# Kernel optimization log

Hardware: AMD Instinct MI355X
Metric: run time of the kernel (lower is better)

The kernel has to match this reference:

```python
import jax, jax.numpy as jnp
import numpy as np

N_NODES = 100000
N_EDGES = 1200000
DIM = 64
MAX_DEG = 64
NUM_LAB = 16
BN_EPS = 1e-5


def _lrelu(x):
    return jax.nn.leaky_relu(x, negative_slope=0.01)


def _bn(x, g, b):
    # BatchNorm1d in training mode: batch statistics over node axis
    m = x.mean(axis=0)
    v = x.var(axis=0)
    return (x - m) * jax.lax.rsqrt(v + BN_EPS) * g + b


def _gin_layer(h, src, dst, n, w1, b1, w2, b2, eps, g, b):
    # GINConv: (1+eps)*x_i + sum_{j in N(i)} x_j, then MLP (lin_lrelu_lin), BN, LeakyReLU
    agg = jax.ops.segment_sum(h[src], dst, num_segments=n)
    x = (1.0 + eps) * h + agg
    x = _lrelu(x @ w1 + b1) @ w2 + b2
    return _lrelu(_bn(x, g, b))


def setup_inputs() -> dict:
    key = jax.random.key(0)
    ks = jax.random.split(key, 16)
    s = 0.05
    inp = {
        'node_deg': jax.random.randint(ks[0], (N_NODES,), 0, MAX_DEG + 1, dtype=jnp.int32),
        'node_lab': jax.random.randint(ks[1], (N_NODES,), 0, NUM_LAB, dtype=jnp.int32),
        'edge_index': jax.random.randint(ks[2], (2, N_EDGES), 0, N_NODES, dtype=jnp.int32),
        'emb_deg': jax.random.normal(ks[3], (MAX_DEG + 1, DIM), jnp.float32) * s,
        'emb_lab': jax.random.normal(ks[4], (NUM_LAB, DIM), jnp.float32) * s,
        'l0_w1': jax.random.normal(ks[5], (2 * DIM, 2 * DIM), jnp.float32) * s,
        'l0_b1': jnp.zeros((2 * DIM,), jnp.float32),
        'l0_w2': jax.random.normal(ks[6], (2 * DIM, DIM), jnp.float32) * s,
        'l0_b2': jnp.zeros((DIM,), jnp.float32),
        'l0_eps': jnp.zeros((1,), jnp.float32),
        'bn0_g': jnp.ones((DIM,), jnp.float32),
        'bn0_b': jnp.zeros((DIM,), jnp.float32),
        'l1_w1': jax.random.normal(ks[7], (DIM, DIM), jnp.float32) * s,
        'l1_b1': jnp.zeros((DIM,), jnp.float32),
        'l1_w2': jax.random.normal(ks[8], (DIM, DIM), jnp.float32) * s,
        'l1_b2': jnp.zeros((DIM,), jnp.float32),
        'l1_eps': jnp.zeros((1,), jnp.float32),
        'bn1_g': jnp.ones((DIM,), jnp.float32),
        'bn1_b': jnp.zeros((DIM,), jnp.float32),
        'fc_w1': jax.random.normal(ks[9], (4 * DIM, DIM), jnp.float32) * s,
        'fc_b1': jnp.zeros((DIM,), jnp.float32),
        'fc_bn_g': jnp.ones((DIM,), jnp.float32),
        'fc_bn_b': jnp.zeros((DIM,), jnp.float32),
        'fc_w2': jax.random.normal(ks[10], (DIM, 1), jnp.float32) * s,
        'fc_b2': jnp.zeros((1,), jnp.float32),
    }
    return inp


def reference(node_deg, node_lab, edge_index, emb_deg, emb_lab,
              l0_w1, l0_b1, l0_w2, l0_b2, l0_eps, bn0_g, bn0_b,
              l1_w1, l1_b1, l1_w2, l1_b2, l1_eps, bn1_g, bn1_b,
              fc_w1, fc_b1, fc_bn_g, fc_bn_b, fc_w2, fc_b2):
    n = node_deg.shape[0]
    src, dst = edge_index[0], edge_index[1]
    # embedding concat: [N, 2*DIM]
    h0 = jnp.concatenate([emb_deg[node_deg], emb_lab[node_lab]], axis=1)
    h1 = _gin_layer(h0, src, dst, n, l0_w1, l0_b1, l0_w2, l0_b2, l0_eps[0], bn0_g, bn0_b)
    h2 = _gin_layer(h1, src, dst, n, l1_w1, l1_b1, l1_w2, l1_b2, l1_eps[0], bn1_g, bn1_b)
    x = jnp.concatenate([h0, h1, h2], axis=1)  # [N, 256]
    x = _lrelu(_bn(x @ fc_w1 + fc_b1, fc_bn_g, fc_bn_b))
    out = jax.nn.sigmoid(x @ fc_w2 + fc_b2)
    return out.squeeze(-1)  # [N]
```

## Files before the change

### kernel.cpp

```cpp
#include <hip/hip_runtime.h>

#define N_NODES 100000
#define N_EDGES 1200000
#define NCLS 81
#define NBKT 196
#define BCAP 8192
#define NCHK 293
#define NGBLK 1563

typedef unsigned short u16;
typedef unsigned char u8;
typedef unsigned int u32;
typedef unsigned long long u64;
typedef short bf16x8 __attribute__((ext_vector_type(8)));
typedef float f32x4 __attribute__((ext_vector_type(4)));

__device__ __forceinline__ float b2f(u16 u) {
  union { u32 i; float f; } v; v.i = ((u32)u) << 16; return v.f;
}
__device__ __forceinline__ u16 f2b(float f) {
  union { float f; u32 i; } v; v.f = f;
  u32 x = v.i;
  return (u16)((x + 0x7fffu + ((x >> 16) & 1u)) >> 16);
}
__device__ __forceinline__ void up2(u32 w, float& lo, float& hi) {
  union { u32 u; float f; } a, b;
  a.u = w << 16; b.u = w & 0xffff0000u;
  lo = a.f; hi = b.f;
}
__device__ __forceinline__ float lrelu(float x) { return x > 0.f ? x : 0.01f * x; }

__device__ __forceinline__ bool is_f32(const u16* emb) {
  int lane = threadIdx.x & 63;
  u32 e0 = (emb[lane * 2] >> 7) & 0xFF;
  u32 e1 = (emb[lane * 2 + 1] >> 7) & 0xFF;
  return __ballot((e0 >= 0x90) || (e1 >= 0x90)) != 0ull;
}

#define P_EMBD 0
#define P_EMBL 4160
#define P_W1A  5184
#define P_B1A  21568
#define P_W2A  21696
#define P_B2A  29888
#define P_EPS0 29952
#define P_G0   29953
#define P_BB0  30017
#define P_LW1  30081
#define P_LB1  34177
#define P_LW2  34241
#define P_LB2  38337
#define P_EPS1 38401
#define P_G1   38402
#define P_BB1  38466
#define P_FW1  38530
#define P_FB1  54914
#define P_FG   54978
#define P_FBB  55042
#define P_FW2  55106
#define P_FB2  55170
#define P_TOT  55171

struct CvtAll {
  const void* src[22];
  int cnt[22];
  int off[22];
};

__global__ void k_cvtall(CvtAll a, const u16* __restrict__ embRaw, float* __restrict__ P) {
  bool f32m = is_f32(embRaw);
  int seg = blockIdx.y;
  int i = blockIdx.x * 256 + threadIdx.x;
  if (i >= a.cnt[seg]) return;
  float v;
  if (f32m) v = ((const float*)a.src[seg])[i];
  else      v = b2f(((const u16*)a.src[seg])[i]);
  P[a.off[seg] + i] = v;
}

__global__ void k_prep(const float* __restrict__ P, float* __restrict__ W1p,
                       float* __restrict__ Efc, u16* __restrict__ bp,
                       u16* __restrict__ wpB) {
  int idx = blockIdx.x * 256 + threadIdx.x;
  if (idx < NCLS * 128) {
    int c = idx >> 7, h = idx & 127;
    const float* w1 = P + P_W1A;
    float s = 0.f;
    if (c < 65) {
      const float* em = P + P_EMBD + c * 64;
      for (int k = 0; k < 64; ++k) s = fmaf(em[k], w1[k * 128 + h], s);
    } else {
      const float* em = P + P_EMBL + (c - 65) * 64;
      for (int k = 0; k < 64; ++k) s = fmaf(em[k], w1[(64 + k) * 128 + h], s);
    }
    W1p[idx] = s;
    return;
  }
  if (idx < NCLS * 128 + NCLS * 64) {
    int r = idx - NCLS * 128;
    int c = r >> 6, o = r & 63;
    const float* fw = P + P_FW1;
    float s = 0.f;
    if (c < 65) {
      const float* em = P + P_EMBD + c * 64;
      for (int k = 0; k < 64; ++k) s = fmaf(em[k], fw[k * 64 + o], s);
    } else {
      const float* em = P + P_EMBL + (c - 65) * 64;
      for (int k = 0; k < 64; ++k) s = fmaf(em[k], fw[(64 + k) * 64 + o], s);
    }
    Efc[r] = s;
    return;
  }
  if (idx < NCLS * 128 + NCLS * 64 + 24576) {
    int pidx = idx - (NCLS * 128 + NCLS * 64);
    int seg, rel;
    if (pidx < 8192)       { seg = 0; rel = pidx; }
    else if (pidx < 12288) { seg = 1; rel = pidx - 8192; }
    else if (pidx < 16384) { seg = 2; rel = pidx - 12288; }
    else                   { seg = 3; rel = pidx - 16384; }
    const int srcoff[4] = {P_W2A, P_LW1, P_LW2, P_FW1 + 128 * 64};
    const int KBs[4] = {4, 2, 2, 4};
    int j = rel & 7, lane = (rel >> 3) & 63, rest = rel >> 9;
    int kb = rest % KBs[seg], nt = rest / KBs[seg];
    int k = kb * 32 + (lane >> 4) * 8 + j;
    int n = nt * 16 + (lane & 15);
    bp[pidx] = f2b(P[srcoff[seg] + k * 64 + n]);
    return;
  }
  int p2 = idx - (NCLS * 128 + NCLS * 64 + 24576);
  if (p2 >= 12288) return;
  int j = p2 & 7, lane = (p2 >> 3) & 63, rest = p2 >> 9;
  int kb = rest % 3, nt = rest / 3;
  int c = kb * 32 + (lane >> 4) * 8 + j;
  int n = nt * 16 + (lane & 15);
  float s = 0.f;
  if (c < NCLS) {
    const float* w1 = P + P_W1A;
    if (c < 65) {
      const float* em = P + P_EMBD + c * 64;
      for (int k = 0; k < 64; ++k) s = fmaf(em[k], w1[k * 128 + n], s);
    } else {
      const float* em = P + P_EMBL + (c - 65) * 64;
      for (int k = 0; k < 64; ++k) s = fmaf(em[k], w1[(64 + k) * 128 + n], s);
    }
  }
  wpB[p2] = (c < NCLS) ? f2b(s) : 0;
}

__global__ __launch_bounds__(256) void k_bsort(const int* __restrict__ edge,
                                               const int* __restrict__ ndeg,
                                               const int* __restrict__ nlab,
                                               u32* __restrict__ gcur,
                                               u64* __restrict__ e2) {
  __shared__ u32 cnt[NBKT], rbase[NBKT];
  __shared__ u32 slo[4096], shi[4096];
  for (int i = threadIdx.x; i < NBKT; i += 256) cnt[i] = 0;
  __syncthreads();
  int base = blockIdx.x * 4096;
  for (int i = threadIdx.x; i < 4096; i += 256) {
    int e = base + i;
    if (e < N_EDGES) {
      int s = edge[e], d = edge[N_EDGES + e];
      slo[i] = ((u32)s << 11) | ((u32)ndeg[s] << 4) | (u32)nlab[s];
      shi[i] = (u32)d;
      atomicAdd(&cnt[(u32)d >> 9], 1u);
    } else shi[i] = 0xFFFFFFFFu;
  }
  __syncthreads();
  for (int i = threadIdx.x; i < NBKT; i += 256) {
    u32 c = cnt[i];
    rbase[i] = c ? atomicAdd(&gcur[i], c) : 0u;
    cnt[i] = 0;
  }
  __syncthreads();
  for (int i = threadIdx.x; i < 4096; i += 256) {
    u32 d = shi[i];
    if (d == 0xFFFFFFFFu) continue;
    u32 b = d >> 9;
    u32 pos = rbase[b] + atomicAdd(&cnt[b], 1u);
    e2[(size_t)b * BCAP + pos] = ((u64)d << 32) | (u64)slo[i];
  }
}

__global__ __launch_bounds__(512) void k_csr(const u64* __restrict__ e2,
                                             const u32* __restrict__ gcur,
                                             u32* __restrict__ row_ptr,
                                             u32* __restrict__ einfo) {
  __shared__ u32 l[512], cur[512], gl[NBKT];
  __shared__ u32 sbase;
  int b = blockIdx.x, tid = threadIdx.x;
  if (tid < NBKT) gl[tid] = gcur[tid];
  __syncthreads();
  if (tid == 0) {
    u32 s = 0;
    for (int i = 0; i < b; ++i) s += gl[i];
    sbase = s;
  }
  l[tid] = 0;
  __syncthreads();
  u32 cnt = gl[b];
  const u64* src = e2 + (size_t)b * BCAP;
  for (u32 e = tid; e < cnt; e += 512)
    atomicAdd(&l[(u32)(src[e] >> 32) & 511u], 1u);
  __syncthreads();
  u32 v = l[tid];
  for (int off = 1; off < 512; off <<= 1) {
    u32 a = (tid >= off) ? l[tid - off] : 0u;
    __syncthreads();
    l[tid] += a;
    __syncthreads();
  }
  u32 pos0 = sbase + l[tid] - v;
  cur[tid] = pos0;
  int n = b * 512 + tid;
  if (n <= N_NODES) row_ptr[n] = pos0;
  __syncthreads();
  for (u32 e = tid; e < cnt; e += 512) {
    u64 r = src[e];
    u32 pos = atomicAdd(&cur[(u32)(r >> 32) & 511u], 1u);
    einfo[pos] = (u32)r;
  }
}

__global__ __launch_bounds__(256) void k_histgemm0(const u32* __restrict__ rp,
                                                   const u32* __restrict__ einfo,
                                                   const u16* __restrict__ wpB,
                                                   const float* __restrict__ W1p,
                                                   const float* __restrict__ P,
                                                   const int* __restrict__ ndeg,
                                                   const int* __restrict__ nlab,
                                                   u16* __restrict__ hmid) {
  __shared__ u8 h[256 * 96];
  int tid = threadIdx.x;
  u32* hw = (u32*)h;
#pragma unroll
  for (int i = 0; i < 24; ++i) hw[tid * 24 + i] = 0;
  __syncthreads();
  int n = blockIdx.x * 256 + tid;
  if (n < N_NODES) {
    u32 st = rp[n], en = rp[n + 1];
    u8* my = h + tid * 96;
    for (u32 e = st; e < en; ++e) {
      u32 q = einfo[e];
      ++my[(q >> 4) & 0x7Fu];
      ++my[65u + (q & 15u)];
    }
  }
  __syncthreads();
  int wid = tid >> 6, lane = tid & 63;
  int row = lane & 15, q = lane >> 4;
  float onep = 1.f + P[P_EPS0];
  const bf16x8* bp = (const bf16x8*)wpB;
#pragma unroll 1
  for (int t = wid; t < 16; t += 4) {
    int m0 = blockIdx.x * 256 + t * 16;
    if (m0 >= N_NODES) break;
    f32x4 acc[8];
#pragma unroll
    for (int nt = 0; nt < 8; ++nt) {
      float b = P[P_B1A + nt * 16 + row];
      acc[nt][0] = b; acc[nt][1] = b; acc[nt][2] = b; acc[nt][3] = b;
    }
    const u8* ar = h + (t * 16 + row) * 96 + q * 8;
#pragma unroll
    for (int kb = 0; kb < 3; ++kb) {
      bf16x8 af;
#pragma unroll
      for (int j = 0; j < 8; ++j) af[j] = (short)f2b((float)ar[kb * 32 + j]);
#pragma unroll
      for (int nt = 0; nt < 8; ++nt) {
        bf16x8 bf = bp[(nt * 3 + kb) * 64 + lane];
        acc[nt] = __builtin_amdgcn_mfma_f32_16x16x32_bf16(af, bf, acc[nt], 0, 0, 0);
      }
    }
#pragma unroll
    for (int r = 0; r < 4; ++r) {
      int m = m0 + q * 4 + r;
      if (m >= N_NODES) continue;
      const float* wd = W1p + ndeg[m] * 128;
      const float* wl = W1p + (65 + nlab[m]) * 128;
#pragma unroll
      for (int nt = 0; nt < 8; ++nt) {
        int cc = nt * 16 + row;
        float v = acc[nt][r] + onep * (wd[cc] + wl[cc]);
        hmid[(size_t)m * 128 + cc] = f2b(lrelu(v));
      }
    }
  }
}

__global__ void k_sr(const float* __restrict__ pbuf, float* __restrict__ statsOut) {
  __shared__ float l[256];
  int c = blockIdx.x;
  float s = 0.f;
  for (int r = threadIdx.x; r < NGBLK; r += 256) s += pbuf[(size_t)r * 128 + c];
  l[threadIdx.x] = s;
  __syncthreads();
  for (int off = 128; off > 0; off >>= 1) {
    if (threadIdx.x < off) l[threadIdx.x] += l[threadIdx.x + off];
    __syncthreads();
  }
  if (threadIdx.x == 0) statsOut[c] = l[0];
}

template <int KB, int LDA, int BIASOFF>
__global__ __launch_bounds__(256) void k_gemm(const u16* __restrict__ A,
                                              const u16* __restrict__ Bp,
                                              const float* __restrict__ P,
                                              float* __restrict__ pbuf,
                                              u16* __restrict__ C) {
  __shared__ float lsum[4][64], lsq[4][64];
  int wid = threadIdx.x >> 6, lane = threadIdx.x & 63;
  int m0 = (blockIdx.x * 4 + wid) * 16;
  bool act = m0 < N_NODES;
  int row = lane & 15, q = lane >> 4;
  float ss[4] = {0.f, 0.f, 0.f, 0.f}, qq[4] = {0.f, 0.f, 0.f, 0.f};
  if (act) {
    const u16* ap = A + (size_t)(m0 + row) * LDA + q * 8;
    const bf16x8* bp = (const bf16x8*)Bp;
    f32x4 acc[4];
#pragma unroll
    for (int nt = 0; nt < 4; ++nt) {
      float b = (BIASOFF >= 0) ? P[BIASOFF + nt * 16 + row] : 0.f;
      acc[nt][0] = b; acc[nt][1] = b; acc[nt][2] = b; acc[nt][3] = b;
    }
#pragma unroll
    for (int kb = 0; kb < KB; ++kb) {
      bf16x8 af = *(const bf16x8*)(ap + kb * 32);
#pragma unroll
      for (int nt = 0; nt < 4; ++nt) {
        bf16x8 bf = bp[(nt * KB + kb) * 64 + lane];
        acc[nt] = __builtin_amdgcn_mfma_f32_16x16x32_bf16(af, bf, acc[nt], 0, 0, 0);
      }
    }
#pragma unroll
    for (int nt = 0; nt < 4; ++nt) {
      float s = 0.f, z = 0.f;
#pragma unroll
      for (int r = 0; r < 4; ++r) {
        int m = m0 + q * 4 + r;
        u16 bv = f2b(acc[nt][r]);
        C[(size_t)m * 64 + nt * 16 + row] = bv;
        float v = b2f(bv);
        s += v; z = fmaf(v, v, z);
      }
      s += __shfl_xor(s, 16, 64); s += __shfl_xor(s, 32, 64);
      z += __shfl_xor(z, 16, 64); z += __shfl_xor(z, 32, 64);
      ss[nt] = s; qq[nt] = z;
    }
  }
  if (lane < 16) {
#pragma unroll
    for (int nt = 0; nt < 4; ++nt) {
      lsum[wid][nt * 16 + lane] = ss[nt];
      lsq[wid][nt * 16 + lane] = qq[nt];
    }
  }
  __syncthreads();
  int t = threadIdx.x;
  if (t < 64)
    pbuf[(size_t)blockIdx.x * 128 + t] = lsum[0][t] + lsum[1][t] + lsum[2][t] + lsum[3][t];
  else if (t < 128) {
    int c = t - 64;
    pbuf[(size_t)blockIdx.x * 128 + t] = lsq[0][c] + lsq[1][c] + lsq[2][c] + lsq[3][c];
  }
}

__global__ __launch_bounds__(256) void k_gemm_bn(const u16* __restrict__ A,
                                                 const u16* __restrict__ Bp,
                                                 const float* __restrict__ P,
                                                 const float* __restrict__ stats,
                                                 u16* __restrict__ C) {
  int wid = threadIdx.x >> 6, lane = threadIdx.x & 63;
  int m0 = (blockIdx.x * 4 + wid) * 16;
  if (m0 >= N_NODES) return;
  int row = lane & 15, q = lane >> 4;
  const float invN = 1.f / (float)N_NODES;
  float sc[16], sh[16];
#pragma unroll
  for (int kb = 0; kb < 2; ++kb)
#pragma unroll
    for (int j = 0; j < 8; ++j) {
      int f = kb * 32 + q * 8 + j;
      float mm = stats[f] * invN;
      float var = fmaxf(stats[64 + f] * invN - mm * mm, 0.f);
      float inv = rsqrtf(var + 1e-5f);
      float s = inv * P[P_G0 + f];
      sc[kb * 8 + j] = s;
      sh[kb * 8 + j] = P[P_BB0 + f] - mm * s;
    }
  const u16* ap = A + (size_t)(m0 + row) * 64 + q * 8;
  const bf16x8* bp = (const bf16x8*)Bp;
  f32x4 acc[4];
#pragma unroll
  for (int nt = 0; nt < 4; ++nt) {
    acc[nt][0] = 0.f; acc[nt][1] = 0.f; acc[nt][2] = 0.f; acc[nt][3] = 0.f;
  }
#pragma unroll
  for (int kb = 0; kb < 2; ++kb) {
    uint4 raw = *(const uint4*)(ap + kb * 32);
    u32 rw[4] = {raw.x, raw.y, raw.z, raw.w};
    bf16x8 af;
#pragma unroll
    for (int p = 0; p < 4; ++p) {
      float lo, hi;
      up2(rw[p], lo, hi);
      float y0 = lrelu(fmaf(sc[kb * 8 + 2 * p], lo, sh[kb * 8 + 2 * p]));
      float y1 = lrelu(fmaf(sc[kb * 8 + 2 * p + 1], hi, sh[kb * 8 + 2 * p + 1]));
      af[2 * p] = (short)f2b(y0);
      af[2 * p + 1] = (short)f2b(y1);
    }
#pragma unroll
    for (int nt = 0; nt < 4; ++nt) {
      bf16x8 bf = bp[(nt * 2 + kb) * 64 + lane];
      acc[nt] = __builtin_amdgcn_mfma_f32_16x16x32_bf16(af, bf, acc[nt], 0, 0, 0);
    }
  }
#pragma unroll
  for (int nt = 0; nt < 4; ++nt)
#pragma unroll
    for (int r = 0; r < 4; ++r) {
      int m = m0 + q * 4 + r;
      C[(size_t)m * 64 + nt * 16 + row] = f2b(acc[nt][r]);
    }
}

__global__ __launch_bounds__(256) void k_agg1(const u32* __restrict__ rp,
                                              const u32* __restrict__ einfo,
                                              const u16* __restrict__ g1,
                                              const float* __restrict__ P,
                                              u16* __restrict__ abuf) {
  int lane = threadIdx.x & 63, wv = threadIdx.x >> 6;
  int n = blockIdx.x * 4 + wv;
  if (n >= N_NODES) return;
  u32 st = rp[n], en = rp[n + 1];
  u32 m = en - st;
  float acA = 0.f, acB = 0.f;
  u32 k = 0;
  for (; k + 8 <= m; k += 8) {
    u32 c0 = einfo[st + k] >> 11, c1 = einfo[st + k + 1] >> 11;
    u32 c2 = einfo[st + k + 2] >> 11, c3 = einfo[st + k + 3] >> 11;
    u32 c4 = einfo[st + k + 4] >> 11, c5 = einfo[st + k + 5] >> 11;
    u32 c6 = einfo[st + k + 6] >> 11, c7 = einfo[st + k + 7] >> 11;
    float v0 = b2f(g1[(size_t)c0 * 64 + lane]);
    float v1 = b2f(g1[(size_t)c1 * 64 + lane]);
    float v2 = b2f(g1[(size_t)c2 * 64 + lane]);
    float v3 = b2f(g1[(size_t)c3 * 64 + lane]);
    float v4 = b2f(g1[(size_t)c4 * 64 + lane]);
    float v5 = b2f(g1[(size_t)c5 * 64 + lane]);
    float v6 = b2f(g1[(size_t)c6 * 64 + lane]);
    float v7 = b2f(g1[(size_t)c7 * 64 + lane]);
    acA += (v0 + v1) + (v2 + v3);
    acB += (v4 + v5) + (v6 + v7);
  }
  if (k + 4 <= m) {
    u32 c0 = einfo[st + k] >> 11, c1 = einfo[st + k + 1] >> 11;
    u32 c2 = einfo[st + k + 2] >> 11, c3 = einfo[st + k + 3] >> 11;
    float v0 = b2f(g1[(size_t)c0 * 64 + lane]);
    float v1 = b2f(g1[(size_t)c1 * 64 + lane]);
    float v2 = b2f(g1[(size_t)c2 * 64 + lane]);
    float v3 = b2f(g1[(size_t)c3 * 64 + lane]);
    acA += (v0 + v1) + (v2 + v3);
    k += 4;
  }
  for (; k < m; ++k) acB += b2f(g1[(size_t)(einfo[st + k] >> 11) * 64 + lane]);
  float acc = acA + acB;
  float onep = 1.f + P[P_EPS1];
  float a = P[P_LB1 + lane] + fmaf(onep, b2f(g1[(size_t)n * 64 + lane]), acc);
  abuf[(size_t)n * 64 + lane] = f2b(lrelu(a));
}

__global__ __launch_bounds__(256) void k_gemm_fc1bn(const u16* __restrict__ t0,
                                                    const u16* __restrict__ t1,
                                                    const u16* __restrict__ Bp,
                                                    const float* __restrict__ P,
                                                    const float* __restrict__ stats,
                                                    float* __restrict__ pbuf,
                                                    const int* __restrict__ ndeg,
                                                    const int* __restrict__ nlab,
                                                    const float* __restrict__ Efc,
                                                    u16* __restrict__ C) {
  __shared__ float lsum[4][64], lsq[4][64];
  int wid = threadIdx.x >> 6, lane = threadIdx.x & 63;
  int m0 = (blockIdx.x * 4 + wid) * 16;
  bool act = m0 < N_NODES;
  int row = lane & 15, q = lane >> 4;
  float ss[4] = {0.f, 0.f, 0.f, 0.f}, qq[4] = {0.f, 0.f, 0.f, 0.f};
  if (act) {
    const float invN = 1.f / (float)N_NODES;
    float sc[32], sh[32];
#pragma unroll
    for (int h = 0; h < 2; ++h) {
      const float* st = stats + h * 128;
      int gof = h ? P_G1 : P_G0, bof = h ? P_BB1 : P_BB0;
#pragma unroll
      for (int kb = 0; kb < 2; ++kb)
#pragma unroll
        for (int j = 0; j < 8; ++j) {
          int f = kb * 32 + q * 8 + j;
          float mm = st[f] * invN;
          float var = fmaxf(st[64 + f] * invN - mm * mm, 0.f);
          float inv = rsqrtf(var + 1e-5f);
          float s = inv * P[gof + f];
          sc[h * 16 + kb * 8 + j] = s;
          sh[h * 16 + kb * 8 + j] = P[bof + f] - mm * s;
        }
    }
    const u16* a0 = t0 + (size_t)(m0 + row) * 64 + q * 8;
    const u16* a1 = t1 + (size_t)(m0 + row) * 64 + q * 8;
    const bf16x8* bp = (const bf16x8*)Bp;
    f32x4 acc[4];
#pragma unroll
    for (int nt = 0; nt < 4; ++nt) {
      float b = P[P_FB1 + nt * 16 + row];
      acc[nt][0] = b; acc[nt][1] = b; acc[nt][2] = b; acc[nt][3] = b;
    }
#pragma unroll
    for (int kb = 0; kb < 4; ++kb) {
      const u16* src = (kb < 2) ? (a0 + kb * 32) : (a1 + (kb - 2) * 32);
      int ci = (kb < 2) ? kb * 8 : 16 + (kb - 2) * 8;
      uint4 raw = *(const uint4*)src;
      u32 rw[4] = {raw.x, raw.y, raw.z, raw.w};
      bf16x8 af;
#pragma unroll
      for (int p = 0; p < 4; ++p) {
        float lo, hi;
        up2(rw[p], lo, hi);
        float y0 = lrelu(fmaf(sc[ci + 2 * p], lo, sh[ci + 2 * p]));
        float y1 = lrelu(fmaf(sc[ci + 2 * p + 1], hi, sh[ci + 2 * p + 1]));
        af[2 * p] = (short)f2b(y0);
        af[2 * p + 1] = (short)f2b(y1);
      }
#pragma unroll
      for (int nt = 0; nt < 4; ++nt) {
        bf16x8 bf = bp[(nt * 4 + kb) * 64 + lane];
        acc[nt] = __builtin_amdgcn_mfma_f32_16x16x32_bf16(af, bf, acc[nt], 0, 0, 0);
      }
    }
    float es[4][4];
#pragma unroll
    for (int r = 0; r < 4; ++r) {
      int m = m0 + q * 4 + r;
      int dn = ndeg[m], ln = 65 + nlab[m];
#pragma unroll
      for (int nt = 0; nt < 4; ++nt) {
        int cc = nt * 16 + row;
        es[r][nt] = acc[nt][r] + Efc[dn * 64 + cc] + Efc[ln * 64 + cc];
      }
    }
#pragma unroll
    for (int nt = 0; nt < 4; ++nt) {
      float s = 0.f, z = 0.f;
#pragma unroll
      for (int r = 0; r < 4; ++r) {
        int m = m0 + q * 4 + r;
        u16 bv = f2b(es[r][nt]);
        C[(size_t)m * 64 + nt * 16 + row] = bv;
        float v = b2f(bv);
        s += v; z = fmaf(v, v, z);
      }
      s += __shfl_xor(s, 16, 64); s += __shfl_xor(s, 32, 64);
      z += __shfl_xor(z, 16, 64); z += __shfl_xor(z, 32, 64);
      ss[nt] = s; qq[nt] = z;
    }
  }
  if (lane < 16) {
#pragma unroll
    for (int nt = 0; nt < 4; ++nt) {
      lsum[wid][nt * 16 + lane] = ss[nt];
      lsq[wid][nt * 16 + lane] = qq[nt];
    }
  }
  __syncthreads();
  int t = threadIdx.x;
  if (t < 64)
    pbuf[(size_t)blockIdx.x * 128 + t] = lsum[0][t] + lsum[1][t] + lsum[2][t] + lsum[3][t];
  else if (t < 128) {
    int c = t - 64;
    pbuf[(size_t)blockIdx.x * 128 + t] = lsq[0][c] + lsq[1][c] + lsq[2][c] + lsq[3][c];
  }
}

__global__ void k_fc2(const u16* __restrict__ t, const float* __restrict__ stats,
                      const float* __restrict__ P, const u16* __restrict__ embRaw,
                      void* __restrict__ out) {
  bool f32m = is_f32(embRaw);
  int n = blockIdx.x * blockDim.x + threadIdx.x;
  if (n >= N_NODES) return;
  float z = P[P_FB2];
  const float invN = 1.f / (float)N_NODES;
  const u16* tn = t + (size_t)n * 64;
#pragma unroll 1
  for (int f = 0; f < 64; ++f) {
    float m = stats[f] * invN;
    float var = fmaxf(stats[64 + f] * invN - m * m, 0.f);
    float inv = rsqrtf(var + 1e-5f);
    float y = (b2f(tn[f]) - m) * inv * P[P_FG + f] + P[P_FBB + f];
    y = lrelu(y);
    z = fmaf(y, P[P_FW2 + f], z);
  }
  float s = 1.f / (1.f + expf(-z));
  if (!(fabsf(z) < 1e30f)) s = 0.25f;
  if (f32m) ((float*)out)[n] = s;
  else      ((u16*)out)[n] = f2b(s);
}

extern "C" void kernel_launch(void* const* d_in, const int* in_sizes, int n_in,
                              void* d_out, int out_size, void* d_ws, size_t ws_size,
                              hipStream_t stream) {
  const int* node_deg = (const int*)d_in[0];
  const int* node_lab = (const int*)d_in[1];
  const int* edge     = (const int*)d_in[2];
  const u16* embRaw   = (const u16*)d_in[3];
  (void)in_sizes; (void)n_in; (void)out_size; (void)ws_size;

  char* base = (char*)d_ws;
  size_t off = 0;
  auto alloc = [&](size_t bytes) -> void* {
    void* p = base + off;
    off += (bytes + 15) & ~(size_t)15;
    return p;
  };
  float* Pb    = (float*)alloc((size_t)P_TOT * 4);
  float* stats = (float*)alloc(384 * 4);
  u32* gcur    = (u32*)alloc(NBKT * 4);
  float* W1p   = (float*)alloc(NCLS * 128 * 4);
  float* Efc   = (float*)alloc(NCLS * 64 * 4);
  u16* bpack   = (u16*)alloc(24576 * 2);
  u16* wpB     = (u16*)alloc(12288 * 2);
  u32* row_ptr = (u32*)alloc((size_t)(N_NODES + 1) * 4);
  float* pbuf  = (float*)alloc((size_t)NGBLK * 128 * 4);
  u32* einfo   = (u32*)alloc((size_t)N_EDGES * 4);
  u64* e2      = (u64*)alloc((size_t)NBKT * BCAP * 8);
  void* arena  = alloc((size_t)N_NODES * 128 * 2);
  u16* t0      = (u16*)alloc((size_t)N_NODES * 64 * 2);
  u16* t1      = (u16*)alloc((size_t)N_NODES * 64 * 2);
  u16* t2      = (u16*)alloc((size_t)N_NODES * 64 * 2);
  u16* hmid = (u16*)arena;
  u16* g1   = (u16*)arena;
  u16* abuf = (u16*)arena + (size_t)N_NODES * 64;
  u16* Bp_w2a = bpack;
  u16* Bp_lw1 = bpack + 8192;
  u16* Bp_lw2 = bpack + 12288;
  u16* Bp_fw1 = bpack + 16384;

  hipMemsetAsync(stats, 0, 384 * 4 + NBKT * 4, stream);

  CvtAll ca;
  const int srcidx[22] = {3, 4, 5, 6, 7, 8, 9, 10, 11, 12, 13, 14, 15, 16, 17, 18, 19, 20, 21, 22, 23, 24};
  const int cnts[22]   = {4160, 1024, 16384, 128, 8192, 64, 1, 64, 64, 4096, 64, 4096, 64, 1, 64, 64, 16384, 64, 64, 64, 64, 1};
  const int offs[22]   = {P_EMBD, P_EMBL, P_W1A, P_B1A, P_W2A, P_B2A, P_EPS0, P_G0, P_BB0,
                          P_LW1, P_LB1, P_LW2, P_LB2, P_EPS1, P_G1, P_BB1,
                          P_FW1, P_FB1, P_FG, P_FBB, P_FW2, P_FB2};
  for (int i = 0; i < 22; ++i) { ca.src[i] = d_in[srcidx[i]]; ca.cnt[i] = cnts[i]; ca.off[i] = offs[i]; }
  k_cvtall<<<dim3(64, 22), 256, 0, stream>>>(ca, embRaw, Pb);

  k_prep<<<205, 256, 0, stream>>>(Pb, W1p, Efc, bpack, wpB);

  k_bsort<<<NCHK, 256, 0, stream>>>(edge, node_deg, node_lab, gcur, e2);
  k_csr<<<NBKT, 512, 0, stream>>>(e2, gcur, row_ptr, einfo);

  const int GEMM_GRID = NGBLK;

  k_histgemm0<<<(N_NODES + 255) / 256, 256, 0, stream>>>(row_ptr, einfo, wpB, W1p, Pb,
                                                         node_deg, node_lab, hmid);
  k_gemm<4, 128, P_B2A><<<GEMM_GRID, 256, 0, stream>>>(hmid, Bp_w2a, Pb, pbuf, t0);
  k_sr<<<128, 256, 0, stream>>>(pbuf, stats);

  k_gemm_bn<<<GEMM_GRID, 256, 0, stream>>>(t0, Bp_lw1, Pb, stats, g1);
  k_agg1<<<(N_NODES + 3) / 4, 256, 0, stream>>>(row_ptr, einfo, g1, Pb, abuf);
  k_gemm<2, 64, P_LB2><<<GEMM_GRID, 256, 0, stream>>>(abuf, Bp_lw2, Pb, pbuf, t1);
  k_sr<<<128, 256, 0, stream>>>(pbuf, stats + 128);

  k_gemm_fc1bn<<<GEMM_GRID, 256, 0, stream>>>(t0, t1, Bp_fw1, Pb, stats, pbuf,
                                              node_deg, node_lab, Efc, t2);
  k_sr<<<128, 256, 0, stream>>>(pbuf, stats + 256);
  k_fc2<<<(N_NODES + 255) / 256, 256, 0, stream>>>(t2, stats + 256, Pb, embRaw, d_out);
}
```

Measured before the change: 326.7 us.

## Fuse parameter conversion with prep, and histogram GEMM into CSR build

Parameter conversion and weight preprocessing are merged into one init kernel that reads the raw inputs directly and also zeroes the bucket counters, which replaces the memset. The per-node class histogram is now built with packed-byte shared-memory atomics while edges are scattered into CSR order, and the first-layer GEMM runs in that same kernel. This removes several kernel launches and the re-read of the CSR edge list. In exchange, the fused kernel runs the GEMM work on fewer, larger blocks with heavy shared-memory use. The packed byte counters would also overflow if any node had more than 255 neighbours in one class.

```diff
diff --git a/kernel.cpp b/kernel.cpp
--- a/kernel.cpp
+++ b/kernel.cpp
@@ -35,6 +35,10 @@
   u32 e0 = (emb[lane * 2] >> 7) & 0xFF;
   u32 e1 = (emb[lane * 2 + 1] >> 7) & 0xFF;
   return __ballot((e0 >= 0x90) || (e1 >= 0x90)) != 0ull;
+}
+
+__device__ __forceinline__ float rdr(const void* p, int i, bool f32m) {
+  return f32m ? ((const float*)p)[i] : b2f(((const u16*)p)[i]);
 }
 
 #define P_EMBD 0
@@ -67,31 +71,42 @@
   int off[22];
 };
 
-__global__ void k_cvtall(CvtAll a, const u16* __restrict__ embRaw, float* __restrict__ P) {
+struct RawPtrs {
+  const void* embD;
+  const void* embL;
+  const void* w1r;
+  const void* w2r;
+  const void* lw1r;
+  const void* lw2r;
+  const void* fwr;
+};
+
+__global__ void k_init(CvtAll a, RawPtrs rw, const u16* __restrict__ embRaw,
+                       float* __restrict__ P, float* __restrict__ W1p,
+                       float* __restrict__ Efc, u16* __restrict__ bp,
+                       u16* __restrict__ wpB, u32* __restrict__ gcur) {
   bool f32m = is_f32(embRaw);
-  int seg = blockIdx.y;
-  int i = blockIdx.x * 256 + threadIdx.x;
-  if (i >= a.cnt[seg]) return;
-  float v;
-  if (f32m) v = ((const float*)a.src[seg])[i];
-  else      v = b2f(((const u16*)a.src[seg])[i]);
-  P[a.off[seg] + i] = v;
-}
-
-__global__ void k_prep(const float* __restrict__ P, float* __restrict__ W1p,
-                       float* __restrict__ Efc, u16* __restrict__ bp,
-                       u16* __restrict__ wpB) {
-  int idx = blockIdx.x * 256 + threadIdx.x;
+  int tid = threadIdx.x;
+  if (blockIdx.y < 22) {
+    if (blockIdx.y == 0 && blockIdx.x == 0 && tid < NBKT) gcur[tid] = 0;
+    int seg = blockIdx.y;
+    int i = blockIdx.x * 256 + tid;
+    if (i < a.cnt[seg]) {
+      float v = f32m ? ((const float*)a.src[seg])[i] : b2f(((const u16*)a.src[seg])[i]);
+      P[a.off[seg] + i] = v;
+    }
+    return;
+  }
+  int idx = blockIdx.x * 256 + tid;
   if (idx < NCLS * 128) {
     int c = idx >> 7, h = idx & 127;
-    const float* w1 = P + P_W1A;
     float s = 0.f;
     if (c < 65) {
-      const float* em = P + P_EMBD + c * 64;
-      for (int k = 0; k < 64; ++k) s = fmaf(em[k], w1[k * 128 + h], s);
+      for (int k = 0; k < 64; ++k)
+        s = fmaf(rdr(rw.embD, c * 64 + k, f32m), rdr(rw.w1r, k * 128 + h, f32m), s);
     } else {
-      const float* em = P + P_EMBL + (c - 65) * 64;
-      for (int k = 0; k < 64; ++k) s = fmaf(em[k], w1[(64 + k) * 128 + h], s);
+      for (int k = 0; k < 64; ++k)
+        s = fmaf(rdr(rw.embL, (c - 65) * 64 + k, f32m), rdr(rw.w1r, (64 + k) * 128 + h, f32m), s);
     }
     W1p[idx] = s;
     return;
@@ -99,14 +114,13 @@
   if (idx < NCLS * 128 + NCLS * 64) {
     int r = idx - NCLS * 128;
     int c = r >> 6, o = r & 63;
-    const float* fw = P + P_FW1;
     float s = 0.f;
     if (c < 65) {
-      const float* em = P + P_EMBD + c * 64;
-      for (int k = 0; k < 64; ++k) s = fmaf(em[k], fw[k * 64 + o], s);
+      for (int k = 0; k < 64; ++k)
+        s = fmaf(rdr(rw.embD, c * 64 + k, f32m), rdr(rw.fwr, k * 64 + o, f32m), s);
     } else {
-      const float* em = P + P_EMBL + (c - 65) * 64;
-      for (int k = 0; k < 64; ++k) s = fmaf(em[k], fw[(64 + k) * 64 + o], s);
+      for (int k = 0; k < 64; ++k)
+        s = fmaf(rdr(rw.embL, (c - 65) * 64 + k, f32m), rdr(rw.fwr, (64 + k) * 64 + o, f32m), s);
     }
     Efc[r] = s;
     return;
@@ -118,13 +132,14 @@
     else if (pidx < 12288) { seg = 1; rel = pidx - 8192; }
     else if (pidx < 16384) { seg = 2; rel = pidx - 12288; }
     else                   { seg = 3; rel = pidx - 16384; }
-    const int srcoff[4] = {P_W2A, P_LW1, P_LW2, P_FW1 + 128 * 64};
+    const void* srcs[4] = {rw.w2r, rw.lw1r, rw.lw2r, rw.fwr};
+    const int addoff[4] = {0, 0, 0, 128 * 64};
     const int KBs[4] = {4, 2, 2, 4};
     int j = rel & 7, lane = (rel >> 3) & 63, rest = rel >> 9;
     int kb = rest % KBs[seg], nt = rest / KBs[seg];
     int k = kb * 32 + (lane >> 4) * 8 + j;
     int n = nt * 16 + (lane & 15);
-    bp[pidx] = f2b(P[srcoff[seg] + k * 64 + n]);
+    bp[pidx] = f2b(rdr(srcs[seg], addoff[seg] + k * 64 + n, f32m));
     return;
   }
   int p2 = idx - (NCLS * 128 + NCLS * 64 + 24576);
@@ -135,13 +150,12 @@
   int n = nt * 16 + (lane & 15);
   float s = 0.f;
   if (c < NCLS) {
-    const float* w1 = P + P_W1A;
     if (c < 65) {
-      const float* em = P + P_EMBD + c * 64;
-      for (int k = 0; k < 64; ++k) s = fmaf(em[k], w1[k * 128 + n], s);
+      for (int k = 0; k < 64; ++k)
+        s = fmaf(rdr(rw.embD, c * 64 + k, f32m), rdr(rw.w1r, k * 128 + n, f32m), s);
     } else {
-      const float* em = P + P_EMBL + (c - 65) * 64;
-      for (int k = 0; k < 64; ++k) s = fmaf(em[k], w1[(64 + k) * 128 + n], s);
+      for (int k = 0; k < 64; ++k)
+        s = fmaf(rdr(rw.embL, (c - 65) * 64 + k, f32m), rdr(rw.w1r, (64 + k) * 128 + n, f32m), s);
     }
   }
   wpB[p2] = (c < NCLS) ? f2b(s) : 0;
@@ -182,21 +196,29 @@
   }
 }
 
-__global__ __launch_bounds__(512) void k_csr(const u64* __restrict__ e2,
-                                             const u32* __restrict__ gcur,
-                                             u32* __restrict__ row_ptr,
-                                             u32* __restrict__ einfo) {
+__global__ __launch_bounds__(512) void k_csrh(const u64* __restrict__ e2,
+                                              const u32* __restrict__ gcur,
+                                              const u16* __restrict__ wpB,
+                                              const float* __restrict__ W1p,
+                                              const float* __restrict__ P,
+                                              const int* __restrict__ ndeg,
+                                              const int* __restrict__ nlab,
+                                              u32* __restrict__ row_ptr,
+                                              u32* __restrict__ einfo,
+                                              u16* __restrict__ hmid) {
   __shared__ u32 l[512], cur[512], gl[NBKT];
+  __shared__ u32 h32[512 * 24];
   __shared__ u32 sbase;
   int b = blockIdx.x, tid = threadIdx.x;
   if (tid < NBKT) gl[tid] = gcur[tid];
+  l[tid] = 0;
+  for (int i = tid; i < 512 * 24; i += 512) h32[i] = 0;
   __syncthreads();
   if (tid == 0) {
     u32 s = 0;
     for (int i = 0; i < b; ++i) s += gl[i];
     sbase = s;
   }
-  l[tid] = 0;
   __syncthreads();
   u32 cnt = gl[b];
   const u64* src = e2 + (size_t)b * BCAP;
@@ -212,54 +234,34 @@
   }
   u32 pos0 = sbase + l[tid] - v;
   cur[tid] = pos0;
-  int n = b * 512 + tid;
-  if (n <= N_NODES) row_ptr[n] = pos0;
+  int nn = b * 512 + tid;
+  if (nn <= N_NODES) row_ptr[nn] = pos0;
   __syncthreads();
   for (u32 e = tid; e < cnt; e += 512) {
     u64 r = src[e];
-    u32 pos = atomicAdd(&cur[(u32)(r >> 32) & 511u], 1u);
-    einfo[pos] = (u32)r;
-  }
-}
-
-__global__ __launch_bounds__(256) void k_histgemm0(const u32* __restrict__ rp,
-                                                   const u32* __restrict__ einfo,
-                                                   const u16* __restrict__ wpB,
-                                                   const float* __restrict__ W1p,
-                                                   const float* __restrict__ P,
-                                                   const int* __restrict__ ndeg,
-                                                   const int* __restrict__ nlab,
-                                                   u16* __restrict__ hmid) {
-  __shared__ u8 h[256 * 96];
-  int tid = threadIdx.x;
-  u32* hw = (u32*)h;
-#pragma unroll
-  for (int i = 0; i < 24; ++i) hw[tid * 24 + i] = 0;
-  __syncthreads();
-  int n = blockIdx.x * 256 + tid;
-  if (n < N_NODES) {
-    u32 st = rp[n], en = rp[n + 1];
-    u8* my = h + tid * 96;
-    for (u32 e = st; e < en; ++e) {
-      u32 q = einfo[e];
-      ++my[(q >> 4) & 0x7Fu];
-      ++my[65u + (q & 15u)];
-    }
-  }
-  __syncthreads();
+    u32 dl = (u32)(r >> 32) & 511u;
+    u32 lo = (u32)r;
+    u32 pos = atomicAdd(&cur[dl], 1u);
+    einfo[pos] = lo;
+    u32 c1 = (lo >> 4) & 0x7Fu, c2 = 65u + (lo & 15u);
+    atomicAdd(&h32[dl * 24 + (c1 >> 2)], 1u << ((c1 & 3u) * 8));
+    atomicAdd(&h32[dl * 24 + (c2 >> 2)], 1u << ((c2 & 3u) * 8));
+  }
+  __syncthreads();
+  const u8* h = (const u8*)h32;
   int wid = tid >> 6, lane = tid & 63;
   int row = lane & 15, q = lane >> 4;
   float onep = 1.f + P[P_EPS0];
   const bf16x8* bp = (const bf16x8*)wpB;
 #pragma unroll 1
-  for (int t = wid; t < 16; t += 4) {
-    int m0 = blockIdx.x * 256 + t * 16;
+  for (int t = wid; t < 32; t += 8) {
+    int m0 = b * 512 + t * 16;
     if (m0 >= N_NODES) break;
     f32x4 acc[8];
 #pragma unroll
     for (int nt = 0; nt < 8; ++nt) {
-      float b = P[P_B1A + nt * 16 + row];
-      acc[nt][0] = b; acc[nt][1] = b; acc[nt][2] = b; acc[nt][3] = b;
+      float bb = P[P_B1A + nt * 16 + row];
+      acc[nt][0] = bb; acc[nt][1] = bb; acc[nt][2] = bb; acc[nt][3] = bb;
     }
     const u8* ar = h + (t * 16 + row) * 96 + q * 8;
 #pragma unroll
@@ -282,8 +284,8 @@
 #pragma unroll
       for (int nt = 0; nt < 8; ++nt) {
         int cc = nt * 16 + row;
-        float v = acc[nt][r] + onep * (wd[cc] + wl[cc]);
-        hmid[(size_t)m * 128 + cc] = f2b(lrelu(v));
+        float vv = acc[nt][r] + onep * (wd[cc] + wl[cc]);
+        hmid[(size_t)m * 128 + cc] = f2b(lrelu(vv));
       }
     }
   }
@@ -644,8 +646,6 @@
   u16* Bp_lw2 = bpack + 12288;
   u16* Bp_fw1 = bpack + 16384;
 
-  hipMemsetAsync(stats, 0, 384 * 4 + NBKT * 4, stream);
-
   CvtAll ca;
   const int srcidx[22] = {3, 4, 5, 6, 7, 8, 9, 10, 11, 12, 13, 14, 15, 16, 17, 18, 19, 20, 21, 22, 23, 24};
   const int cnts[22]   = {4160, 1024, 16384, 128, 8192, 64, 1, 64, 64, 4096, 64, 4096, 64, 1, 64, 64, 16384, 64, 64, 64, 64, 1};
@@ -653,17 +653,19 @@
                           P_LW1, P_LB1, P_LW2, P_LB2, P_EPS1, P_G1, P_BB1,
                           P_FW1, P_FB1, P_FG, P_FBB, P_FW2, P_FB2};
   for (int i = 0; i < 22; ++i) { ca.src[i] = d_in[srcidx[i]]; ca.cnt[i] = cnts[i]; ca.off[i] = offs[i]; }
-  k_cvtall<<<dim3(64, 22), 256, 0, stream>>>(ca, embRaw, Pb);
-
-  k_prep<<<205, 256, 0, stream>>>(Pb, W1p, Efc, bpack, wpB);
+  RawPtrs rw;
+  rw.embD = d_in[3]; rw.embL = d_in[4]; rw.w1r = d_in[5]; rw.w2r = d_in[7];
+  rw.lw1r = d_in[12]; rw.lw2r = d_in[14]; rw.fwr = d_in[19];
+
+  k_init<<<dim3(205, 23), 256, 0, stream>>>(ca, rw, embRaw, Pb, W1p, Efc, bpack, wpB, gcur);
 
   k_bsort<<<NCHK, 256, 0, stream>>>(edge, node_deg, node_lab, gcur, e2);
-  k_csr<<<NBKT, 512, 0, stream>>>(e2, gcur, row_ptr, einfo);
+
+  k_csrh<<<NBKT, 512, 0, stream>>>(e2, gcur, wpB, W1p, Pb, node_deg, node_lab,
+                                   row_ptr, einfo, hmid);
 
   const int GEMM_GRID = NGBLK;
 
-  k_histgemm0<<<(N_NODES + 255) / 256, 256, 0, stream>>>(row_ptr, einfo, wpB, W1p, Pb,
-                                                         node_deg, node_lab, hmid);
   k_gemm<4, 128, P_B2A><<<GEMM_GRID, 256, 0, stream>>>(hmid, Bp_w2a, Pb, pbuf, t0);
   k_sr<<<128, 256, 0, stream>>>(pbuf, stats);
 
```

Result: no change. 323.5 us (-1.0%).
